# Optimization experiments

Hardware: AMD Instinct MI355X
Metric: run time of the kernel (lower is better)

Reference implementation:

```python
import jax, jax.numpy as jnp
import numpy as np
from jax import lax

THRESH = 0.6      # pnet score threshold (threshold[0])
IOU_THR = 0.5     # per-scale nms threshold in detect_face
K_PICKS = 128     # fixed max number of NMS picks (jit-static)
STRIDE = 2.0
CELL = 12.0
NEG = -1e30


def _conv(x, w, b):
    y = lax.conv_general_dilated(x, w, (1, 1), 'VALID',
                                 dimension_numbers=('NCHW', 'OIHW', 'NCHW'))
    return y + b[None, :, None, None]


def _prelu(x, a):
    return jnp.where(x > 0, x, a[None, :, None, None] * x)


def _maxpool2(x):
    return lax.reduce_window(x, -jnp.inf, lax.max, (1, 1, 2, 2), (1, 1, 2, 2), 'VALID')


def _nms(boxes, scores):
    # Greedy union-IoU NMS (nms_numpy math), vectorized with a fixed pick budget.
    # boxes [N,4] (shared grid), scores [N] with invalid entries already = NEG.
    x1, y1, x2, y2 = boxes[:, 0], boxes[:, 1], boxes[:, 2], boxes[:, 3]
    area = (x2 - x1 + 1.0) * (y2 - y1 + 1.0)

    def body(live, _):
        j = jnp.argmax(live)
        s = live[j]
        ok = s > NEG * 0.5
        xx1 = jnp.maximum(x1[j], x1); yy1 = jnp.maximum(y1[j], y1)
        xx2 = jnp.minimum(x2[j], x2); yy2 = jnp.minimum(y2[j], y2)
        inter = jnp.maximum(0.0, xx2 - xx1 + 1.0) * jnp.maximum(0.0, yy2 - yy1 + 1.0)
        iou = inter / (area[j] + area - inter)
        live = jnp.where(iou > IOU_THR, NEG, live).at[j].set(NEG)
        return live, (j, ok)

    _, (idx, ok) = lax.scan(body, scores, None, length=K_PICKS)
    return idx, ok


def setup_inputs():
    key = jax.random.key(0)
    ks = jax.random.split(key, 16)
    B, H, W = 16, 384, 512
    f = lambda k, shp, s=0.1: jax.random.normal(k, shp, jnp.float32) * s
    return {
        'im_data': jax.random.uniform(ks[0], (B, 3, H, W), jnp.float32) * 255.0,
        'c1_w': f(ks[1], (10, 3, 3, 3)), 'c1_b': f(ks[2], (10,)),
        'p1': jnp.full((10,), 0.25, jnp.float32),
        'c2_w': f(ks[3], (16, 10, 3, 3)), 'c2_b': f(ks[4], (16,)),
        'p2': jnp.full((16,), 0.25, jnp.float32),
        'c3_w': f(ks[5], (32, 16, 3, 3)), 'c3_b': f(ks[6], (32,)),
        'p3': jnp.full((32,), 0.25, jnp.float32),
        'c41_w': f(ks[7], (2, 32, 1, 1)), 'c41_b': f(ks[8], (2,)),
        'c42_w': f(ks[9], (4, 32, 1, 1)), 'c42_b': f(ks[10], (4,)),
    }


def reference(im_data, c1_w, c1_b, p1, c2_w, c2_b, p2, c3_w, c3_b, p3,
              c41_w, c41_b, c42_w, c42_b):
    # --- PNet conv trunk (detect_face normalization + MTCNN PNet) ---
    x = (im_data - 127.5) * 0.0078125
    h = _prelu(_conv(x, c1_w, c1_b), p1)
    h = _maxpool2(h)                                   # 2x2 s2 (dims even -> ceil==floor)
    h = _prelu(_conv(h, c2_w, c2_b), p2)
    h = _prelu(_conv(h, c3_w, c3_b), p3)
    probs = jax.nn.softmax(_conv(h, c41_w, c41_b), axis=1)[:, 1]   # [B,Hp,Wp]
    reg = _conv(h, c42_w, c42_b)                                   # [B,4,Hp,Wp]

    # --- generateBoundingBox (dense, masked instead of nonzero; scale=1) ---
    B, Hp, Wp = probs.shape
    yy, xx = jnp.meshgrid(jnp.arange(Hp, dtype=jnp.float32),
                          jnp.arange(Wp, dtype=jnp.float32), indexing='ij')
    boxes4 = jnp.stack([jnp.floor(STRIDE * xx + 1.0).ravel(),
                        jnp.floor(STRIDE * yy + 1.0).ravel(),
                        jnp.floor(STRIDE * xx + CELL).ravel(),
                        jnp.floor(STRIDE * yy + CELL).ravel()], axis=1)  # [N,4]
    scores = probs.reshape(B, -1)                                   # [B,N]
    regf = reg.reshape(B, 4, -1).transpose(0, 2, 1)                 # [B,N,4]
    masked = jnp.where(scores >= THRESH, scores, NEG)

    # --- per-image greedy NMS (batched_nms: images independent) ---
    idx, ok = jax.vmap(_nms, in_axes=(None, 0))(boxes4, masked)     # [B,K]
    pb = boxes4[idx]                                                # [B,K,4]
    ps = jnp.take_along_axis(scores, idx, axis=1)                   # [B,K]
    pr = jnp.take_along_axis(regf, idx[..., None], axis=1)          # [B,K,4]

    w = pb[..., 2] - pb[..., 0]
    hh = pb[..., 3] - pb[..., 1]
    q1 = pb[..., 0] + pr[..., 0] * w
    q2 = pb[..., 1] + pr[..., 1] * hh
    q3 = pb[..., 2] + pr[..., 2] * w
    q4 = pb[..., 3] + pr[..., 3] * hh
    rw = q3 - q1
    rh = q4 - q2
    l = jnp.maximum(rw, rh)
    nx1 = q1 + rw * 0.5 - l * 0.5
    ny1 = q2 + rh * 0.5 - l * 0.5
    out = jnp.stack([nx1, ny1, nx1 + l, ny1 + l, ps], axis=-1)      # [B,K,5]
    return out * ok[..., None].astype(out.dtype)
```

## Files before the change

### kernel.cpp

```cpp
#include <hip/hip_runtime.h>
#include <math.h>

#define BATCH 16
#define IH 384
#define IW 512
#define C1 10
#define P1H 191
#define P1W 255
#define C2 16
#define H2 189
#define W2 253
#define C3 32
#define H3 187
#define W3 251
#define N3 (H3*W3)
#define KP 128
#define CAP 7680
#define NEGV (-1e30f)

typedef _Float16 f16x8 __attribute__((ext_vector_type(8)));
typedef _Float16 f16x4 __attribute__((ext_vector_type(4)));
typedef float    f32x16 __attribute__((ext_vector_type(16)));

#define PXT 66
#define NSUB 2

__global__ __launch_bounds__(256, 2) void k_conv1pool(
        const float* __restrict__ im, const float* __restrict__ w,
        const float* __restrict__ bia, const float* __restrict__ slope,
        float* __restrict__ outp,
        const float* __restrict__ w3, _Float16* __restrict__ wbuf) {
    if (blockIdx.x == 0 && blockIdx.y == 0 && blockIdx.z == 0) {
        int tid = threadIdx.y * 16 + threadIdx.x;
        for (int e = tid; e < 4608; e += 256) {
            int oc = e / 144;
            int rem = e - oc * 144;
            int ic = rem / 9;
            int tap = rem - ic * 9;
            float v = w3[e];
            _Float16 h = (_Float16)v;
            _Float16 l = (_Float16)(v - (float)h);
            int d = ((tap * 2 + (ic >> 3)) * 32 + oc) * 8 + (ic & 7);
            wbuf[d] = h;
            wbuf[4608 + d] = l;
        }
    }

    int x = blockIdx.x * 16 + threadIdx.x;
    int y = blockIdx.y * 16 + threadIdx.y;
    int bb = blockIdx.z;
    if (x >= P1W || y >= P1H) return;

    float in[3][4][4];
    #pragma unroll
    for (int ci = 0; ci < 3; ++ci) {
        const float* p = im + (((size_t)bb * 3 + ci) * IH + 2 * y) * IW + 2 * x;
        #pragma unroll
        for (int r = 0; r < 4; ++r) {
            const float2* q = (const float2*)(p + (size_t)r * IW);
            float2 a0 = q[0], a1 = q[1];
            in[ci][r][0] = a0.x; in[ci][r][1] = a0.y;
            in[ci][r][2] = a1.x; in[ci][r][3] = a1.y;
        }
    }
    #pragma unroll
    for (int ci = 0; ci < 3; ++ci)
        #pragma unroll
        for (int r = 0; r < 4; ++r)
            #pragma unroll
            for (int c = 0; c < 4; ++c)
                in[ci][r][c] = (in[ci][r][c] - 127.5f) * 0.0078125f;

    #pragma unroll
    for (int oc = 0; oc < C1; ++oc) {
        const float* wo = w + oc * 27;
        float bv = bia[oc], sv = slope[oc];
        float best = -INFINITY;
        #pragma unroll
        for (int py = 0; py < 2; ++py)
            #pragma unroll
            for (int px = 0; px < 2; ++px) {
                float acc = bv;
                #pragma unroll
                for (int ci = 0; ci < 3; ++ci)
                    #pragma unroll
                    for (int ky = 0; ky < 3; ++ky)
                        #pragma unroll
                        for (int kx = 0; kx < 3; ++kx)
                            acc += in[ci][py + ky][px + kx] * wo[(ci * 3 + ky) * 3 + kx];
                float v = acc > 0.f ? acc : sv * acc;
                best = fmaxf(best, v);
            }
        outp[(((size_t)bb * C1 + oc) * P1H + y) * P1W + x] = best;
    }
}

__global__ __launch_bounds__(256, 2) void k_conv2(
        const float* __restrict__ inp, const float* __restrict__ w,
        const float* __restrict__ bia, const float* __restrict__ slope,
        float* __restrict__ outp) {
    __shared__ float4 sbuf[2048];
    int tx = threadIdx.x, ty = threadIdx.y;
    int tid = ty * 64 + tx;
    int x0 = blockIdx.x * 128 + tx * 2;
    int y  = blockIdx.y * 4 + ty;
    int bb = blockIdx.z;
    bool alive = (x0 < W2) && (y < H2);

    float a0[C2], a1[C2];
    #pragma unroll
    for (int oc = 0; oc < C2; ++oc) { a0[oc] = bia[oc]; a1[oc] = bia[oc]; }

    if (alive) {
        bool tail = (x0 + 3 > P1W - 1);
        for (int ci = 0; ci < C1; ++ci) {
            const float* p = inp + (((size_t)bb * C1 + ci) * P1H + y) * P1W + x0;
            float v[3][4];
            #pragma unroll
            for (int r = 0; r < 3; ++r) {
                const float* pr = p + (size_t)r * P1W;
                v[r][0] = pr[0]; v[r][1] = pr[1]; v[r][2] = pr[2];
                v[r][3] = tail ? 0.f : pr[3];
            }
            const float* wc = w + ci * 9;
            #pragma unroll
            for (int oc = 0; oc < C2; ++oc) {
                const float* wo = wc + oc * (C1 * 9);
                float s0 = a0[oc], s1 = a1[oc];
                #pragma unroll
                for (int ky = 0; ky < 3; ++ky)
                    #pragma unroll
                    for (int kx = 0; kx < 3; ++kx) {
                        float wv = wo[ky * 3 + kx];
                        s0 += v[ky][kx]     * wv;
                        s1 += v[ky][kx + 1] * wv;
                    }
                a0[oc] = s0; a1[oc] = s1;
            }
        }
        #pragma unroll
        for (int oc = 0; oc < C2; ++oc) {
            float sl = slope[oc];
            float u0 = a0[oc]; a0[oc] = u0 > 0.f ? u0 : sl * u0;
            float u1 = a1[oc]; a1[oc] = u1 > 0.f ? u1 : sl * u1;
        }
    }

    #pragma unroll
    for (int c4 = 0; c4 < 4; ++c4) {
        int g0 = tid * 8 + c4;
        int p0 = g0 ^ ((g0 >> 3) & 7);
        sbuf[p0] = make_float4(a0[c4 * 4], a0[c4 * 4 + 1], a0[c4 * 4 + 2], a0[c4 * 4 + 3]);
        int g1 = tid * 8 + 4 + c4;
        int p1 = g1 ^ ((g1 >> 3) & 7);
        sbuf[p1] = make_float4(a1[c4 * 4], a1[c4 * 4 + 1], a1[c4 * 4 + 2], a1[c4 * 4 + 3]);
    }
    __syncthreads();

    const size_t obase = (size_t)bb * H2 * W2 * C2;
    #pragma unroll
    for (int it = 0; it < 8; ++it) {
        int g = it * 256 + tid;
        int c4 = g & 3, px = (g >> 2) & 127, ry = g >> 9;
        int xg = blockIdx.x * 128 + px, yg = blockIdx.y * 4 + ry;
        if (xg < W2 && yg < H2) {
            int phys = g ^ ((g >> 3) & 7);
            *(float4*)(outp + obase + ((size_t)yg * W2 + xg) * C2 + c4 * 4) = sbuf[phys];
        }
    }
}

__global__ __launch_bounds__(256, 2) void k_conv3mfma(
        const float* __restrict__ act,
        const _Float16* __restrict__ wbuf,
        const float* __restrict__ b3, const float* __restrict__ s3,
        const float* __restrict__ w41, const float* __restrict__ b41,
        const float* __restrict__ w42, const float* __restrict__ b42,
        float* __restrict__ scores, float4* __restrict__ regf) {
    __shared__ __align__(16) _Float16 Ah[6 * 2 * PXT * 8];
    __shared__ __align__(16) _Float16 Al[6 * 2 * PXT * 8];
    __shared__ __align__(16) float    htab[32 * 8];

    int tid = threadIdx.x;
    int bx = blockIdx.x * (NSUB * 32);
    int by = blockIdx.y * 4;
    int bb = blockIdx.z;

    {
        int oc = tid >> 3, f = tid & 7;
        float v;
        if      (f == 0) v = b3[oc];
        else if (f == 1) v = s3[oc];
        else if (f == 2) v = w41[oc];
        else if (f == 3) v = w41[32 + oc];
        else             v = w42[(f - 4) * 32 + oc];
        htab[tid] = v;
    }
    {
        const float* actb = act + (size_t)bb * H2 * W2 * C2;
        for (int e = tid; e < 6 * PXT * 4; e += 256) {
            int ic4 = e & 3;
            int t = e >> 2;
            int px = t % PXT;
            int row = t / PXT;
            int yg = by + row, xg = bx + px;
            float4 v = make_float4(0.f, 0.f, 0.f, 0.f);
            if (yg < H2 && xg < W2)
                v = *(const float4*)(actb + ((size_t)yg * W2 + xg) * C2 + ic4 * 4);
            float xs0 = v.x, xs1 = v.y, xs2 = v.z, xs3 = v.w;
            f16x4 hv, lv;
            _Float16 h;
            h = (_Float16)xs0; hv[0] = h; lv[0] = (_Float16)(xs0 - (float)h);
            h = (_Float16)xs1; hv[1] = h; lv[1] = (_Float16)(xs1 - (float)h);
            h = (_Float16)xs2; hv[2] = h; lv[2] = (_Float16)(xs2 - (float)h);
            h = (_Float16)xs3; hv[3] = h; lv[3] = (_Float16)(xs3 - (float)h);
            int kg = ic4 >> 1, h4 = ic4 & 1;
            int gr = (row * 2 + kg) * PXT + px;
            *(f16x4*)(Ah + gr * 8 + h4 * 4) = hv;
            *(f16x4*)(Al + gr * 8 + h4 * 4) = lv;
        }
    }
    __syncthreads();

    int wv = tid >> 6, lane = tid & 63;
    int col = lane & 31, half = lane >> 5;
    int y = by + wv;
    if (y >= H3) return;

    f32x16 acc[NSUB];
    #pragma unroll
    for (int s = 0; s < NSUB; ++s)
        #pragma unroll
        for (int i = 0; i < 16; ++i) acc[s][i] = 0.f;

    const _Float16* wg = wbuf + (half * 32 + col) * 8;

    #pragma unroll 1
    for (int ky = 0; ky < 3; ++ky) {
        const _Float16* arh = Ah + ((wv + ky) * 2 + half) * (PXT * 8);
        const _Float16* arl = Al + ((wv + ky) * 2 + half) * (PXT * 8);
        #pragma unroll
        for (int kx = 0; kx < 3; ++kx) {
            int tap = ky * 3 + kx;
            f16x8 wh = *(const f16x8*)(wg + tap * 512);
            f16x8 wl = *(const f16x8*)(wg + 4608 + tap * 512);
            #pragma unroll
            for (int s = 0; s < NSUB; ++s) {
                int p = s * 32 + col + kx;
                f16x8 bh = *(const f16x8*)(arh + p * 8);
                f16x8 bl = *(const f16x8*)(arl + p * 8);
                acc[s] = __builtin_amdgcn_mfma_f32_32x32x16_f16(wh, bh, acc[s], 0, 0, 0);
                acc[s] = __builtin_amdgcn_mfma_f32_32x32x16_f16(wl, bh, acc[s], 0, 0, 0);
                acc[s] = __builtin_amdgcn_mfma_f32_32x32x16_f16(wh, bl, acc[s], 0, 0, 0);
            }
        }
    }

    float L0[NSUB], L1[NSUB], R0[NSUB], R1[NSUB], R2[NSUB], R3[NSUB];
    #pragma unroll
    for (int s = 0; s < NSUB; ++s) { L0[s]=0.f; L1[s]=0.f; R0[s]=0.f; R1[s]=0.f; R2[s]=0.f; R3[s]=0.f; }

    #pragma unroll
    for (int r = 0; r < 16; ++r) {
        int oc = (r & 3) + 8 * (r >> 2) + 4 * half;
        float4 t0 = *(const float4*)&htab[oc * 8];
        float4 t1 = *(const float4*)&htab[oc * 8 + 4];
        #pragma unroll
        for (int s = 0; s < NSUB; ++s) {
            float v = acc[s][r] + t0.x;
            v = v > 0.f ? v : v * t0.y;
            L0[s] += v * t0.z; L1[s] += v * t0.w;
            R0[s] += v * t1.x; R1[s] += v * t1.y;
            R2[s] += v * t1.z; R3[s] += v * t1.w;
        }
    }

    float hb0 = b41[0], hb1 = b41[1];
    float rb0 = b42[0], rb1 = b42[1], rb2 = b42[2], rb3 = b42[3];

    #pragma unroll
    for (int s = 0; s < NSUB; ++s) {
        float l0 = L0[s] + __shfl_xor(L0[s], 32) + hb0;
        float l1 = L1[s] + __shfl_xor(L1[s], 32) + hb1;
        float r0 = R0[s] + __shfl_xor(R0[s], 32) + rb0;
        float r1 = R1[s] + __shfl_xor(R1[s], 32) + rb1;
        float r2 = R2[s] + __shfl_xor(R2[s], 32) + rb2;
        float r3 = R3[s] + __shfl_xor(R3[s], 32) + rb3;
        float m = fmaxf(l0, l1);
        float e0 = expf(l0 - m), e1 = expf(l1 - m);
        float p = e1 / (e0 + e1);
        int px = bx + s * 32 + col;
        if (half == 0 && px < W3) {
            size_t n = (size_t)bb * N3 + (size_t)y * W3 + px;
            scores[n] = (p >= 0.6f) ? p : NEGV;
            regf[n] = make_float4(r0, r1, r2, r3);
        }
    }
}

__global__ __launch_bounds__(1024) void k_nms(
        const float* __restrict__ scores, const float4* __restrict__ regf,
        float* __restrict__ outp) {
    __shared__ float s_score[CAP];
    __shared__ int   s_idx[CAP];
    __shared__ float r_s[16];
    __shared__ int   r_i[16];
    __shared__ float s_picks[KP];
    __shared__ int   s_picki[KP];
    __shared__ int   s_misc[4];

    int tid = threadIdx.x;
    int bb = blockIdx.x;
    const float* sc = scores + (size_t)bb * N3;

    if (tid < 4) s_misc[tid] = 0;
    __syncthreads();

    int cnt = 0;
    for (int i = tid; i < N3; i += 1024) if (sc[i] > 0.f) cnt++;
    atomicAdd(&s_misc[0], cnt);
    __syncthreads();
    int M = s_misc[0];

    int cutbin = 0;
    if (M > CAP) {
        for (int i = tid; i < 2048; i += 1024) s_idx[i] = 0;
        __syncthreads();
        for (int i = tid; i < N3; i += 1024) {
            float s = sc[i];
            if (s > 0.f) {
                int b = (int)((s - 0.6f) * 5120.f);
                b = b < 0 ? 0 : (b > 2047 ? 2047 : b);
                atomicAdd(&s_idx[b], 1);
            }
        }
        __syncthreads();
        if (tid == 0) {
            int accum = 0, b = 2047;
            for (; b >= 0; --b) {
                int c = s_idx[b];
                if (accum + c > CAP) break;
                accum += c;
            }
            s_misc[2] = b + 1;
        }
        __syncthreads();
        cutbin = s_misc[2];
        __syncthreads();
    }

    for (int i = tid; i < N3; i += 1024) {
        float s = sc[i];
        if (s > 0.f) {
            bool keep = true;
            if (M > CAP) {
                int b = (int)((s - 0.6f) * 5120.f);
                b = b < 0 ? 0 : (b > 2047 ? 2047 : b);
                keep = (b >= cutbin);
            }
            if (keep) {
                int pos = atomicAdd(&s_misc[1], 1);
                if (pos < CAP) { s_score[pos] = s; s_idx[pos] = i; }
            }
        }
    }
    __syncthreads();
    int M2 = s_misc[1]; if (M2 > CAP) M2 = CAP;

    int np = 0;
    for (int pick = 0; pick < KP; ++pick) {
        float bs = -INFINITY; int bi = 0x7fffffff;
        for (int i = tid; i < M2; i += 1024) {
            float s = s_score[i]; int id = s_idx[i];
            if (s > bs || (s == bs && id < bi)) { bs = s; bi = id; }
        }
        #pragma unroll
        for (int off = 32; off; off >>= 1) {
            float os = __shfl_down(bs, off);
            int   oi = __shfl_down(bi, off);
            if (os > bs || (os == bs && oi < bi)) { bs = os; bi = oi; }
        }
        int lane = tid & 63, wv = tid >> 6;
        if (lane == 0) { r_s[wv] = bs; r_i[wv] = bi; }
        __syncthreads();
        if (tid == 0) {
            float ps = r_s[0]; int pi = r_i[0];
            for (int k = 1; k < 16; ++k) {
                float os = r_s[k]; int oi = r_i[k];
                if (os > ps || (os == ps && oi < pi)) { ps = os; pi = oi; }
            }
            s_picks[pick] = ps; s_picki[pick] = pi;
            r_s[0] = ps; r_i[0] = pi;
        }
        __syncthreads();
        float ps = r_s[0]; int pi = r_i[0];
        if (ps < 0.f) break;
        np = pick + 1;

        int pcx = pi % W3, pcy = pi / W3;
        float px1 = (float)(2 * pcx + 1), py1 = (float)(2 * pcy + 1);
        float px2 = (float)(2 * pcx + 12), py2 = (float)(2 * pcy + 12);
        for (int i = tid; i < M2; i += 1024) {
            float s = s_score[i];
            if (s > NEGV * 0.5f) {
                int id = s_idx[i];
                int cx = id % W3, cy = id / W3;
                float x1 = (float)(2 * cx + 1), y1 = (float)(2 * cy + 1);
                float x2 = (float)(2 * cx + 12), y2 = (float)(2 * cy + 12);
                float xx1 = fmaxf(px1, x1), yy1 = fmaxf(py1, y1);
                float xx2 = fminf(px2, x2), yy2 = fminf(py2, y2);
                float inter = fmaxf(0.f, xx2 - xx1 + 1.f) * fmaxf(0.f, yy2 - yy1 + 1.f);
                float iou = inter / (288.f - inter);
                if (iou > 0.5f) s_score[i] = NEGV;
            }
        }
        __syncthreads();
    }

    if (tid < KP) {
        float* o = outp + ((size_t)bb * KP + tid) * 5;
        if (tid < np) {
            int pi = s_picki[tid]; float ps = s_picks[tid];
            int cx = pi % W3, cy = pi / W3;
            float x1 = (float)(2 * cx + 1), y1 = (float)(2 * cy + 1);
            float x2 = (float)(2 * cx + 12), y2 = (float)(2 * cy + 12);
            float4 r = regf[(size_t)bb * N3 + pi];
            float wd = x2 - x1, hh = y2 - y1;
            float q1 = x1 + r.x * wd, q2 = y1 + r.y * hh;
            float q3 = x2 + r.z * wd, q4 = y2 + r.w * hh;
            float rw = q3 - q1, rh = q4 - q2;
            float L = fmaxf(rw, rh);
            float nx1 = q1 + rw * 0.5f - L * 0.5f;
            float ny1 = q2 + rh * 0.5f - L * 0.5f;
            o[0] = nx1; o[1] = ny1; o[2] = nx1 + L; o[3] = ny1 + L; o[4] = ps;
        } else {
            o[0] = 0.f; o[1] = 0.f; o[2] = 0.f; o[3] = 0.f; o[4] = 0.f;
        }
    }
}

extern "C" void kernel_launch(void* const* d_in, const int* in_sizes, int n_in,
                              void* d_out, int out_size, void* d_ws, size_t ws_size,
                              hipStream_t stream) {
    const float* im   = (const float*)d_in[0];
    const float* c1w  = (const float*)d_in[1];
    const float* c1b  = (const float*)d_in[2];
    const float* p1   = (const float*)d_in[3];
    const float* c2w  = (const float*)d_in[4];
    const float* c2b  = (const float*)d_in[5];
    const float* p2   = (const float*)d_in[6];
    const float* c3w  = (const float*)d_in[7];
    const float* c3b  = (const float*)d_in[8];
    const float* p3   = (const float*)d_in[9];
    const float* c41w = (const float*)d_in[10];
    const float* c41b = (const float*)d_in[11];
    const float* c42w = (const float*)d_in[12];
    const float* c42b = (const float*)d_in[13];

    float* ws = (float*)d_ws;
    const size_t POOL1_FLOATS = (size_t)BATCH * C1 * P1H * P1W;
    float*  pool1  = ws;
    float*  conv2b = ws + POOL1_FLOATS;
    float*  scoresb = ws;
    float4* regfb   = (float4*)(ws + (size_t)BATCH * N3);
    _Float16* wbuf = (_Float16*)d_out;

    k_conv1pool<<<dim3(16, 12, BATCH), dim3(16, 16), 0, stream>>>(im, c1w, c1b, p1, pool1,
                                                                  c3w, wbuf);
    k_conv2   <<<dim3(2, 48, BATCH), dim3(64, 4), 0, stream>>>(pool1, c2w, c2b, p2, conv2b);
    k_conv3mfma<<<dim3(4, 47, BATCH), dim3(256), 0, stream>>>(conv2b, wbuf, c3b, p3,
                                                              c41w, c41b, c42w, c42b,
                                                              scoresb, regfb);
    k_nms<<<dim3(BATCH), dim3(1024), 0, stream>>>(scoresb, regfb, (float*)d_out);
}
```

Baseline: 223.7 us.

## Stage conv1 input tile in LDS and compute two pooled outputs per thread

The conv1+maxpool kernel now loads a normalized 3x34x68 input tile into shared memory cooperatively, then each thread computes two adjacent pooled outputs from a register window. This removes redundant overlapping global loads, shares weight loads across eight accumulators, and halves the grid's x dimension. PReLU is applied once after the 2x2 max rather than per conv output. That reordering is only equivalent when the slope is non-negative. It adds LDS use and a barrier per block.

```diff
diff --git a/kernel.cpp b/kernel.cpp
--- a/kernel.cpp
+++ b/kernel.cpp
@@ -25,13 +25,20 @@
 #define PXT 66
 #define NSUB 2
 
+#define T1R 34
+#define T1C 68
 __global__ __launch_bounds__(256, 2) void k_conv1pool(
         const float* __restrict__ im, const float* __restrict__ w,
         const float* __restrict__ bia, const float* __restrict__ slope,
         float* __restrict__ outp,
         const float* __restrict__ w3, _Float16* __restrict__ wbuf) {
-    if (blockIdx.x == 0 && blockIdx.y == 0 && blockIdx.z == 0) {
-        int tid = threadIdx.y * 16 + threadIdx.x;
+    __shared__ float T[3 * T1R * T1C];
+
+    int tx = threadIdx.x, ty = threadIdx.y;
+    int tid = ty * 16 + tx;
+    int bx = blockIdx.x, by = blockIdx.y, bb = blockIdx.z;
+
+    if (bx == 0 && by == 0 && bb == 0) {
         for (int e = tid; e < 4608; e += 256) {
             int oc = e / 144;
             int rem = e - oc * 144;
@@ -46,52 +53,70 @@
         }
     }
 
-    int x = blockIdx.x * 16 + threadIdx.x;
-    int y = blockIdx.y * 16 + threadIdx.y;
-    int bb = blockIdx.z;
-    if (x >= P1W || y >= P1H) return;
-
-    float in[3][4][4];
-    #pragma unroll
-    for (int ci = 0; ci < 3; ++ci) {
-        const float* p = im + (((size_t)bb * 3 + ci) * IH + 2 * y) * IW + 2 * x;
+    const size_t ibase = (size_t)bb * 3 * IH * IW;
+    for (int g = tid; g < 3 * T1R * 33; g += 256) {
+        int ch = g / (T1R * 33);
+        int rem = g - ch * (T1R * 33);
+        int r = rem / 33;
+        int c2 = rem - r * 33;
+        int yg = 32 * by + r;
+        int xg = 64 * bx + 2 * c2;
+        float2 v = make_float2(0.f, 0.f);
+        if (yg < IH && xg < IW)
+            v = *(const float2*)(im + ibase + ((size_t)ch * IH + yg) * IW + xg);
+        float2 o;
+        o.x = (v.x - 127.5f) * 0.0078125f;
+        o.y = (v.y - 127.5f) * 0.0078125f;
+        *(float2*)&T[(ch * T1R + r) * T1C + 2 * c2] = o;
+    }
+    __syncthreads();
+
+    int Y  = by * 16 + ty;
+    int X0 = bx * 32 + 2 * tx;
+    if (Y >= P1H) return;
+
+    float win[3][4][6];
+    #pragma unroll
+    for (int ch = 0; ch < 3; ++ch)
         #pragma unroll
         for (int r = 0; r < 4; ++r) {
-            const float2* q = (const float2*)(p + (size_t)r * IW);
-            float2 a0 = q[0], a1 = q[1];
-            in[ci][r][0] = a0.x; in[ci][r][1] = a0.y;
-            in[ci][r][2] = a1.x; in[ci][r][3] = a1.y;
-        }
-    }
-    #pragma unroll
-    for (int ci = 0; ci < 3; ++ci)
-        #pragma unroll
-        for (int r = 0; r < 4; ++r)
-            #pragma unroll
-            for (int c = 0; c < 4; ++c)
-                in[ci][r][c] = (in[ci][r][c] - 127.5f) * 0.0078125f;
-
-    #pragma unroll
+            const float* p = &T[(ch * T1R + 2 * ty + r) * T1C + 4 * tx];
+            float4 a = *(const float4*)p;
+            float2 b = *(const float2*)(p + 4);
+            win[ch][r][0] = a.x; win[ch][r][1] = a.y;
+            win[ch][r][2] = a.z; win[ch][r][3] = a.w;
+            win[ch][r][4] = b.x; win[ch][r][5] = b.y;
+        }
+
+    bool px1ok = (X0 + 1 < P1W);
     for (int oc = 0; oc < C1; ++oc) {
         const float* wo = w + oc * 27;
         float bv = bia[oc], sv = slope[oc];
-        float best = -INFINITY;
-        #pragma unroll
-        for (int py = 0; py < 2; ++py)
+        float c0 = bv, c1 = bv, c2 = bv, c3 = bv;
+        float c4 = bv, c5 = bv, c6 = bv, c7 = bv;
+        #pragma unroll
+        for (int ch = 0; ch < 3; ++ch)
             #pragma unroll
-            for (int px = 0; px < 2; ++px) {
-                float acc = bv;
+            for (int ky = 0; ky < 3; ++ky)
                 #pragma unroll
-                for (int ci = 0; ci < 3; ++ci)
-                    #pragma unroll
-                    for (int ky = 0; ky < 3; ++ky)
-                        #pragma unroll
-                        for (int kx = 0; kx < 3; ++kx)
-                            acc += in[ci][py + ky][px + kx] * wo[(ci * 3 + ky) * 3 + kx];
-                float v = acc > 0.f ? acc : sv * acc;
-                best = fmaxf(best, v);
-            }
-        outp[(((size_t)bb * C1 + oc) * P1H + y) * P1W + x] = best;
+                for (int kx = 0; kx < 3; ++kx) {
+                    float wv = wo[(ch * 3 + ky) * 3 + kx];
+                    c0 += win[ch][0 + ky][0 + kx] * wv;
+                    c1 += win[ch][0 + ky][1 + kx] * wv;
+                    c2 += win[ch][0 + ky][2 + kx] * wv;
+                    c3 += win[ch][0 + ky][3 + kx] * wv;
+                    c4 += win[ch][1 + ky][0 + kx] * wv;
+                    c5 += win[ch][1 + ky][1 + kx] * wv;
+                    c6 += win[ch][1 + ky][2 + kx] * wv;
+                    c7 += win[ch][1 + ky][3 + kx] * wv;
+                }
+        float m0 = fmaxf(fmaxf(c0, c1), fmaxf(c4, c5));
+        float m1 = fmaxf(fmaxf(c2, c3), fmaxf(c6, c7));
+        float p0 = m0 > 0.f ? m0 : sv * m0;
+        float p1 = m1 > 0.f ? m1 : sv * m1;
+        float* o = outp + (((size_t)bb * C1 + oc) * P1H + Y) * P1W + X0;
+        o[0] = p0;
+        if (px1ok) o[1] = p1;
     }
 }
 
@@ -465,8 +490,8 @@
     float4* regfb   = (float4*)(ws + (size_t)BATCH * N3);
     _Float16* wbuf = (_Float16*)d_out;
 
-    k_conv1pool<<<dim3(16, 12, BATCH), dim3(16, 16), 0, stream>>>(im, c1w, c1b, p1, pool1,
-                                                                  c3w, wbuf);
+    k_conv1pool<<<dim3(8, 12, BATCH), dim3(16, 16), 0, stream>>>(im, c1w, c1b, p1, pool1,
+                                                                 c3w, wbuf);
     k_conv2   <<<dim3(2, 48, BATCH), dim3(64, 4), 0, stream>>>(pool1, c2w, c2b, p2, conv2b);
     k_conv3mfma<<<dim3(4, 47, BATCH), dim3(256), 0, stream>>>(conv2b, wbuf, c3b, p3,
                                                               c41w, c41b, c42w, c42b,
```

Result: slower. 234.8 us (+5.0%).
